# Optimization experiments

Measured on AMD Instinct MI355X. Metric: run time of the kernel, lower is better.

Reference implementation:

```python
import jax, jax.numpy as jnp
import numpy as np

B, N, D, E, MULT = 4, 512, 1024, 8, 4
H = D * MULT
CAPACITY_FACTOR = 1.0
EPSILON = 1e-6


def setup_inputs() -> dict:
    key = jax.random.key(0)
    ks = jax.random.split(key, 4)
    s1 = 1.0 / np.sqrt(D)
    s2 = 1.0 / np.sqrt(H)
    return {
        "x": jax.random.normal(ks[0], (B, N, D), jnp.float32),
        "w_gate": jax.random.uniform(ks[1], (D, E), jnp.float32, -s1, s1),
        "b_gate": jnp.zeros((E,), jnp.float32),
        "w1": jax.random.uniform(ks[2], (E, D, H), jnp.float32, -s1, s1),
        "b1": jnp.zeros((E, H), jnp.float32),
        "w2": jax.random.uniform(ks[3], (E, H, D), jnp.float32, -s2, s2),
        "b2": jnp.zeros((E, D), jnp.float32),
    }


def _cv_squared(v):
    # torch: x.float().var() is unbiased (ddof=1)
    eps = 1e-10
    m = jnp.mean(v)
    return jnp.var(v, ddof=1) / (m * m + eps)


def reference(x, w_gate, b_gate, w1, b1, w2, b2):
    b, n, d = x.shape
    e = w_gate.shape[1]
    capacity = float(int(CAPACITY_FACTOR * b))  # int(capacity_factor * x.size(0))

    # SwitchGate
    gate = jax.nn.softmax(x @ w_gate + b_gate, axis=-1)          # [B,N,E]
    top_idx = jnp.argmax(gate, axis=-1)                          # [B,N]  == topk(1) indices
    # faithful to torch scatter_(dim=1, top_k_indices, 1): mask[bi, idx[bi,ni,0], 0] = 1
    mask = jnp.zeros_like(gate).at[jnp.arange(b)[:, None], top_idx, 0].set(1.0)
    masked = gate * mask
    denom = masked.sum(0, keepdims=True) + EPSILON               # [1,N,E]
    gate_scores = masked / denom * capacity                      # [B,N,E]
    importance = gate_scores.sum(0)                              # [N,E]
    load = (gate_scores > 0).sum(0).astype(jnp.float32)          # [N,E]
    loss = _cv_squared(importance) + _cv_squared(load)

    # Experts: FeedForward(dim, dim, mult) = Linear -> GELU(exact) -> Linear, all E at once
    h = jax.nn.gelu(jnp.einsum('bnd,edh->bneh', x, w1) + b1, approximate=False)  # [B,N,E,H]
    expert_out = jnp.einsum('bneh,ehd->bned', h, w2) + b2                        # [B,N,E,D]

    # moe_output = sum(gate_scores.unsqueeze(-2) * stacked_expert_outputs, dim=-1)
    out = jnp.einsum('bne,bned->bnd', gate_scores, expert_out)                   # [B,N,D]
    return out, loss
```

## Files before the change

kernel.cpp:

```cpp
#include <hip/hip_runtime.h>
#include <math.h>

static constexpr int Bb = 4;
static constexpr int Nn = 512;
static constexpr int Dd = 1024;
static constexpr int Ee = 8;
static constexpr int Hh = 4096;
static constexpr float CAP = 4.0f;
static constexpr float EPS = 1e-6f;

static constexpr int P1S = 32;
static constexpr int P2S = 32;


__global__ __launch_bounds__(256) void k1_gate_ffn1(
    const float* __restrict__ x, const float* __restrict__ wg,
    const float* __restrict__ bg, const float* __restrict__ w1,
    int* __restrict__ bmask, float* __restrict__ gate0,
    float* __restrict__ p1, float* __restrict__ out)
{
    __shared__ float smem[8 * 1028 + 16];
    const int blk = blockIdx.x;
    const int tid = threadIdx.x;

    if (blk < 256) {
        const int hc = blk & 7, ks = blk >> 3, k0 = ks * 32;
        {
            const int t = tid >> 3, q = tid & 7;
            const int row = (t >> 3) * Nn + (t & 7);
            float4 v = *(const float4*)(x + (size_t)row * Dd + k0 + q * 4);
            smem[(q * 4 + 0) * 32 + t] = v.x;
            smem[(q * 4 + 1) * 32 + t] = v.y;
            smem[(q * 4 + 2) * 32 + t] = v.z;
            smem[(q * 4 + 3) * 32 + t] = v.w;
        }
        __syncthreads();
        const int h = hc * 512 + tid * 2;
        const float* wp = w1 + (size_t)k0 * Hh + h;
        float2 acc[32];
#pragma unroll
        for (int t = 0; t < 32; ++t) acc[t] = make_float2(0.f, 0.f);
#pragma unroll
        for (int half = 0; half < 2; ++half) {
            float2 wbuf[16];
#pragma unroll
            for (int kk = 0; kk < 16; ++kk)
                wbuf[kk] = *(const float2*)(wp + (size_t)(half * 16 + kk) * Hh);
#pragma unroll
            for (int kk = 0; kk < 16; ++kk) {
                const float4* xrow = (const float4*)(smem + (half * 16 + kk) * 32);
                const float2 w = wbuf[kk];
#pragma unroll
                for (int t4 = 0; t4 < 8; ++t4) {
                    float4 xv = xrow[t4];
                    acc[t4 * 4 + 0].x = fmaf(xv.x, w.x, acc[t4 * 4 + 0].x);
                    acc[t4 * 4 + 0].y = fmaf(xv.x, w.y, acc[t4 * 4 + 0].y);
                    acc[t4 * 4 + 1].x = fmaf(xv.y, w.x, acc[t4 * 4 + 1].x);
                    acc[t4 * 4 + 1].y = fmaf(xv.y, w.y, acc[t4 * 4 + 1].y);
                    acc[t4 * 4 + 2].x = fmaf(xv.z, w.x, acc[t4 * 4 + 2].x);
                    acc[t4 * 4 + 2].y = fmaf(xv.z, w.y, acc[t4 * 4 + 2].y);
                    acc[t4 * 4 + 3].x = fmaf(xv.w, w.x, acc[t4 * 4 + 3].x);
                    acc[t4 * 4 + 3].y = fmaf(xv.w, w.y, acc[t4 * 4 + 3].y);
                }
            }
        }
        float* o = p1 + ((size_t)ks * 32) * Hh + h;
#pragma unroll
        for (int t = 0; t < 32; ++t) { *(float2*)o = acc[t]; o += Hh; }
    } else if (blk < 512) {
        const int g = blk - 256;
        for (int i = tid; i < Dd * Ee; i += 256)
            smem[(i & 7) * 1028 + (i >> 3)] = wg[i];
        int* bb = (int*)&smem[8224];
        __syncthreads();
        const int wave = tid >> 6, lane = tid & 63;
        for (int j = 0; j < 2; ++j) {
            const int sub = wave + 4 * j;
            const int tok = g * 8 + sub;
            const float* xr = x + (size_t)tok * Dd;
            float acc[Ee];
#pragma unroll
            for (int e = 0; e < Ee; ++e) acc[e] = 0.f;
#pragma unroll
            for (int jj = 0; jj < 4; ++jj) {
                const int d0 = jj * 256 + lane * 4;
                float4 xv = *(const float4*)(xr + d0);
#pragma unroll
                for (int e = 0; e < Ee; ++e) {
                    float4 wv = *(const float4*)(&smem[e * 1028 + d0]);
                    acc[e] = fmaf(xv.x, wv.x, acc[e]);
                    acc[e] = fmaf(xv.y, wv.y, acc[e]);
                    acc[e] = fmaf(xv.z, wv.z, acc[e]);
                    acc[e] = fmaf(xv.w, wv.w, acc[e]);
                }
            }
#pragma unroll
            for (int e = 0; e < Ee; ++e) {
                float v = acc[e];
#pragma unroll
                for (int off = 32; off > 0; off >>= 1) v += __shfl_xor(v, off, 64);
                acc[e] = v + bg[e];
            }
            if (lane == 0) {
                int best = 0;
                float bv = acc[0];
#pragma unroll
                for (int e = 1; e < Ee; ++e)
                    if (acc[e] > bv) { bv = acc[e]; best = e; }
                bb[sub] = 1 << best;
                const int n = tok & (Nn - 1);
                const int b = tok >> 9;
                if (n < 8) {
                    float m = acc[0];
#pragma unroll
                    for (int e = 1; e < Ee; ++e) m = fmaxf(m, acc[e]);
                    float s = 0.f;
#pragma unroll
                    for (int e = 0; e < Ee; ++e) s += expf(acc[e] - m);
                    gate0[b * 8 + n] = expf(acc[0] - m) / s;
                }
            }
        }
        __syncthreads();
        if (tid == 0) {
            int m = 0;
#pragma unroll
            for (int i = 0; i < 8; ++i) m |= bb[i];
            bmask[g] = m;
        }
    } else {
        const int z = blk - 512;
        const float4 zero4 = make_float4(0.f, 0.f, 0.f, 0.f);
#pragma unroll
        for (int r = 0; r < 8; ++r) {
            const int row = z * 8 + r;
            const int n = row & (Nn - 1);
            if (n >= 8)
                *(float4*)(out + (size_t)row * Dd + tid * 4) = zero4;
        }
    }
}

__global__ __launch_bounds__(128) void k2_gelu_score(
    const float* __restrict__ p1, const float* __restrict__ b1,
    float* __restrict__ hT, const int* __restrict__ bmask,
    const float* __restrict__ gate0, float* __restrict__ gs,
    float* __restrict__ loss_out)
{
    const int blk = blockIdx.x, tid = threadIdx.x;
    if (blk < 256) {
        const int idx = blk * 128 + tid;
        const int hh0 = (idx << 2) & (Hh - 1);
        const int t = idx >> 10;
        float4 s = *(const float4*)(b1 + hh0);
#pragma unroll
        for (int q = 0; q < P1S; ++q) {
            float4 v = *(const float4*)(p1 + ((size_t)(q * 32 + t)) * Hh + hh0);
            s.x += v.x; s.y += v.y; s.z += v.z; s.w += v.w;
        }
        const float c = 0.70710678118654752440f;
        float4 r;
        r.x = 0.5f * s.x * (1.f + erff(s.x * c));
        r.y = 0.5f * s.y * (1.f + erff(s.y * c));
        r.z = 0.5f * s.z * (1.f + erff(s.z * c));
        r.w = 0.5f * s.w * (1.f + erff(s.w * c));
        *(float4*)(hT + (size_t)t * Hh + hh0) = r;
    } else if (tid < 64) {
        const int l = tid;
        int m0 = bmask[l], m1 = bmask[64 + l], m2 = bmask[128 + l], m3 = bmask[192 + l];
#pragma unroll
        for (int off = 32; off > 0; off >>= 1) {
            m0 |= __shfl_xor(m0, off, 64);
            m1 |= __shfl_xor(m1, off, 64);
            m2 |= __shfl_xor(m2, off, 64);
            m3 |= __shfl_xor(m3, off, 64);
        }
        float gm = 0.f;
        if (l < 32) {
            const int b = l >> 3, n = l & 7;
            const int sm = (b == 0) ? m0 : (b == 1) ? m1 : (b == 2) ? m2 : m3;
            if ((sm >> n) & 1) gm = gate0[l];
        }
        float den = gm + __shfl_xor(gm, 8, 64);
        den += __shfl_xor(den, 16, 64);
        float gsv = 0.f;
        if (l < 32) { gsv = gm / (den + EPS) * CAP; gs[l] = gsv; }
        float impn = gsv + __shfl_xor(gsv, 8, 64); impn += __shfl_xor(impn, 16, 64);
        float ldv = (gsv > 0.f) ? 1.f : 0.f;
        float ldn = ldv + __shfl_xor(ldv, 8, 64); ldn += __shfl_xor(ldn, 16, 64);
        float si = gsv, sl = ldv;
#pragma unroll
        for (int off = 32; off > 0; off >>= 1) {
            si += __shfl_xor(si, off, 64);
            sl += __shfl_xor(sl, off, 64);
        }
        const float M = (float)(Nn * Ee);
        const float mi = si / M, ml = sl / M;
        float di = (l < 8) ? (impn - mi) * (impn - mi) : 0.f;
        float dl = (l < 8) ? (ldn - ml) * (ldn - ml) : 0.f;
#pragma unroll
        for (int off = 32; off > 0; off >>= 1) {
            di += __shfl_xor(di, off, 64);
            dl += __shfl_xor(dl, off, 64);
        }
        if (l == 0) {
            di += (M - 8.f) * mi * mi;
            dl += (M - 8.f) * ml * ml;
            const float vi = di / (M - 1.f), vl = dl / (M - 1.f);
            *loss_out = vi / (mi * mi + 1e-10f) + vl / (ml * ml + 1e-10f);
        }
    }
}

__global__ __launch_bounds__(128) void k3_ffn2(
    const float* __restrict__ w2, const float* __restrict__ hT,
    float* __restrict__ p2)
{
    __shared__ float smem[128 * 32];
    const int tid = threadIdx.x;
    const int ky = blockIdx.y;
    {
        const int t = tid & 31, kq = tid >> 5;
        const float* src = hT + (size_t)t * Hh + ky * 128 + kq * 32;
#pragma unroll
        for (int c = 0; c < 8; ++c) {
            float4 v = *(const float4*)(src + c * 4);
            smem[(kq * 32 + c * 4 + 0) * 32 + t] = v.x;
            smem[(kq * 32 + c * 4 + 1) * 32 + t] = v.y;
            smem[(kq * 32 + c * 4 + 2) * 32 + t] = v.z;
            smem[(kq * 32 + c * 4 + 3) * 32 + t] = v.w;
        }
    }
    __syncthreads();
    const int d = blockIdx.x * 128 + tid;
    const int k0 = ky * 128;
    const float* wp = w2 + (size_t)k0 * Dd + d;
    float acc[32];
#pragma unroll
    for (int t = 0; t < 32; ++t) acc[t] = 0.f;
#pragma unroll
    for (int q = 0; q < 8; ++q) {
        float wbuf[16];
#pragma unroll
        for (int kk = 0; kk < 16; ++kk)
            wbuf[kk] = wp[(size_t)(q * 16 + kk) * Dd];
#pragma unroll
        for (int kk = 0; kk < 16; ++kk) {
            const float4* xrow = (const float4*)(smem + (q * 16 + kk) * 32);
            const float w = wbuf[kk];
#pragma unroll
            for (int t4 = 0; t4 < 8; ++t4) {
                float4 xv = xrow[t4];
                acc[t4 * 4 + 0] = fmaf(xv.x, w, acc[t4 * 4 + 0]);
                acc[t4 * 4 + 1] = fmaf(xv.y, w, acc[t4 * 4 + 1]);
                acc[t4 * 4 + 2] = fmaf(xv.z, w, acc[t4 * 4 + 2]);
                acc[t4 * 4 + 3] = fmaf(xv.w, w, acc[t4 * 4 + 3]);
            }
        }
    }
    float* o = p2 + ((size_t)ky * 32) * Dd + d;
#pragma unroll
    for (int t = 0; t < 32; ++t) { *o = acc[t]; o += Dd; }
}

__global__ __launch_bounds__(128) void k4_out(
    const float* __restrict__ p2, const float* __restrict__ b2,
    const float* __restrict__ gs, float* __restrict__ out)
{
    const int t = blockIdx.x >> 1;
    const int d4 = (blockIdx.x & 1) * 512 + threadIdx.x * 4;
    float4 a = make_float4(0.f, 0.f, 0.f, 0.f);
    const float* p = p2 + (size_t)t * Dd + d4;
#pragma unroll 8
    for (int s = 0; s < P2S; ++s) {
        float4 v = *(const float4*)p;
        p += (size_t)32 * Dd;
        a.x += v.x; a.y += v.y; a.z += v.z; a.w += v.w;
    }
    float4 bbv = *(const float4*)(b2 + d4);
    const float g = gs[t];
    const int b = t >> 3, n = t & 7;
    float4 o;
    o.x = g * (a.x + bbv.x);
    o.y = g * (a.y + bbv.y);
    o.z = g * (a.z + bbv.z);
    o.w = g * (a.w + bbv.w);
    *(float4*)(out + ((size_t)(b * Nn + n)) * Dd + d4) = o;
}

extern "C" void kernel_launch(void* const* d_in, const int* in_sizes, int n_in,
                              void* d_out, int out_size, void* d_ws, size_t ws_size,
                              hipStream_t stream) {
    const float* x  = (const float*)d_in[0];
    const float* wg = (const float*)d_in[1];
    const float* bg = (const float*)d_in[2];
    const float* w1 = (const float*)d_in[3];
    const float* b1 = (const float*)d_in[4];
    const float* w2 = (const float*)d_in[5];
    const float* b2 = (const float*)d_in[6];
    float* out = (float*)d_out;
    float* wsf = (float*)d_ws;

    int*   bmask = (int*)d_ws;
    float* gate0 = wsf + 256;
    float* gs    = wsf + 320;
    float* hT    = wsf + 512;
    float* p1    = wsf + 132096;
    float* p2    = wsf + 4326400;

    k1_gate_ffn1<<<dim3(768), dim3(256), 0, stream>>>(x, wg, bg, w1, bmask, gate0, p1, out);
    k2_gelu_score<<<dim3(257), dim3(128), 0, stream>>>(p1, b1, hT, bmask, gate0, gs,
                                                       out + (out_size - 1));
    k3_ffn2<<<dim3(8, 32), dim3(128), 0, stream>>>(w2, hT, p2);
    k4_out<<<dim3(64), dim3(128), 0, stream>>>(p2, b2, gs, out);
}
```

Before: 266.5 us.

## Replace split-K FFN1 with full-K register-prefetched tiles and fuse bias+GELU

After: 270.5 us. Within noise of the previous version (+1.5%).

```diff
diff --git a/kernel.cpp b/kernel.cpp
--- a/kernel.cpp
+++ b/kernel.cpp
@@ -1,7 +1,6 @@
 #include <hip/hip_runtime.h>
 #include <math.h>
 
-static constexpr int Bb = 4;
 static constexpr int Nn = 512;
 static constexpr int Dd = 1024;
 static constexpr int Ee = 8;
@@ -9,66 +8,110 @@
 static constexpr float CAP = 4.0f;
 static constexpr float EPS = 1e-6f;
 
-static constexpr int P1S = 32;
 static constexpr int P2S = 32;
 
 
-__global__ __launch_bounds__(256) void k1_gate_ffn1(
+__global__ __launch_bounds__(256) void n1_gate_ffn1(
     const float* __restrict__ x, const float* __restrict__ wg,
     const float* __restrict__ bg, const float* __restrict__ w1,
-    int* __restrict__ bmask, float* __restrict__ gate0,
-    float* __restrict__ p1, float* __restrict__ out)
+    const float* __restrict__ b1, int* __restrict__ bmask,
+    float* __restrict__ gate0, float* __restrict__ hT,
+    float* __restrict__ out)
 {
     __shared__ float smem[8 * 1028 + 16];
     const int blk = blockIdx.x;
     const int tid = threadIdx.x;
 
     if (blk < 256) {
-        const int hc = blk & 7, ks = blk >> 3, k0 = ks * 32;
+        float* sX = smem;
+        float* sW = smem + 2048;
+        const int hb = blk * 16;
+        const int h  = tid & 15;
+        const int tp = tid >> 4;
+        const int t0 = tid & 31, kq = tid >> 5;
+        const int row0 = (t0 >> 3) * Nn + (t0 & 7);
+        const int kwr  = tid >> 4;
+
+        float4 xr0, xr1;
+        float  wr[4];
         {
-            const int t = tid >> 3, q = tid & 7;
-            const int row = (t >> 3) * Nn + (t & 7);
-            float4 v = *(const float4*)(x + (size_t)row * Dd + k0 + q * 4);
-            smem[(q * 4 + 0) * 32 + t] = v.x;
-            smem[(q * 4 + 1) * 32 + t] = v.y;
-            smem[(q * 4 + 2) * 32 + t] = v.z;
-            smem[(q * 4 + 3) * 32 + t] = v.w;
+            const float* xp = x + (size_t)row0 * Dd;
+            xr0 = *(const float4*)(xp + kq * 4);
+            xr1 = *(const float4*)(xp + (kq + 8) * 4);
+#pragma unroll
+            for (int j = 0; j < 4; ++j)
+                wr[j] = w1[(size_t)(kwr + j * 16) * Hh + hb + h];
+        }
+        {
+            sX[(kq * 4 + 0) * 32 + t0] = xr0.x;
+            sX[(kq * 4 + 1) * 32 + t0] = xr0.y;
+            sX[(kq * 4 + 2) * 32 + t0] = xr0.z;
+            sX[(kq * 4 + 3) * 32 + t0] = xr0.w;
+            sX[((kq + 8) * 4 + 0) * 32 + t0] = xr1.x;
+            sX[((kq + 8) * 4 + 1) * 32 + t0] = xr1.y;
+            sX[((kq + 8) * 4 + 2) * 32 + t0] = xr1.z;
+            sX[((kq + 8) * 4 + 3) * 32 + t0] = xr1.w;
+#pragma unroll
+            for (int j = 0; j < 4; ++j)
+                sW[(kwr + j * 16) * 16 + h] = wr[j];
         }
         __syncthreads();
-        const int h = hc * 512 + tid * 2;
-        const float* wp = w1 + (size_t)k0 * Hh + h;
-        float2 acc[32];
-#pragma unroll
-        for (int t = 0; t < 32; ++t) acc[t] = make_float2(0.f, 0.f);
-#pragma unroll
-        for (int half = 0; half < 2; ++half) {
-            float2 wbuf[16];
-#pragma unroll
-            for (int kk = 0; kk < 16; ++kk)
-                wbuf[kk] = *(const float2*)(wp + (size_t)(half * 16 + kk) * Hh);
-#pragma unroll
-            for (int kk = 0; kk < 16; ++kk) {
-                const float4* xrow = (const float4*)(smem + (half * 16 + kk) * 32);
-                const float2 w = wbuf[kk];
-#pragma unroll
-                for (int t4 = 0; t4 < 8; ++t4) {
-                    float4 xv = xrow[t4];
-                    acc[t4 * 4 + 0].x = fmaf(xv.x, w.x, acc[t4 * 4 + 0].x);
-                    acc[t4 * 4 + 0].y = fmaf(xv.x, w.y, acc[t4 * 4 + 0].y);
-                    acc[t4 * 4 + 1].x = fmaf(xv.y, w.x, acc[t4 * 4 + 1].x);
-                    acc[t4 * 4 + 1].y = fmaf(xv.y, w.y, acc[t4 * 4 + 1].y);
-                    acc[t4 * 4 + 2].x = fmaf(xv.z, w.x, acc[t4 * 4 + 2].x);
-                    acc[t4 * 4 + 2].y = fmaf(xv.z, w.y, acc[t4 * 4 + 2].y);
-                    acc[t4 * 4 + 3].x = fmaf(xv.w, w.x, acc[t4 * 4 + 3].x);
-                    acc[t4 * 4 + 3].y = fmaf(xv.w, w.y, acc[t4 * 4 + 3].y);
-                }
-            }
-        }
-        float* o = p1 + ((size_t)ks * 32) * Hh + h;
-#pragma unroll
-        for (int t = 0; t < 32; ++t) { *(float2*)o = acc[t]; o += Hh; }
-    } else if (blk < 512) {
+
+        const float b1v = b1[hb + h];
+        float a0 = b1v, a1 = b1v;
+
+        for (int c = 0; c < 16; ++c) {
+            float4 nx0, nx1;
+            float  nw[4];
+            if (c < 15) {
+                const int k0 = (c + 1) * 64;
+                const float* xp = x + (size_t)row0 * Dd + k0;
+                nx0 = *(const float4*)(xp + kq * 4);
+                nx1 = *(const float4*)(xp + (kq + 8) * 4);
+#pragma unroll
+                for (int j = 0; j < 4; ++j)
+                    nw[j] = w1[(size_t)(k0 + kwr + j * 16) * Hh + hb + h];
+            }
+            const float* xp = sX + 2 * tp;
+#pragma unroll
+            for (int kk = 0; kk < 64; ++kk) {
+                const float  w  = sW[kk * 16 + h];
+                const float2 xv = *(const float2*)(xp + kk * 32);
+                a0 = fmaf(xv.x, w, a0);
+                a1 = fmaf(xv.y, w, a1);
+            }
+            if (c < 15) {
+                __syncthreads();
+                sX[(kq * 4 + 0) * 32 + t0] = nx0.x;
+                sX[(kq * 4 + 1) * 32 + t0] = nx0.y;
+                sX[(kq * 4 + 2) * 32 + t0] = nx0.z;
+                sX[(kq * 4 + 3) * 32 + t0] = nx0.w;
+                sX[((kq + 8) * 4 + 0) * 32 + t0] = nx1.x;
+                sX[((kq + 8) * 4 + 1) * 32 + t0] = nx1.y;
+                sX[((kq + 8) * 4 + 2) * 32 + t0] = nx1.z;
+                sX[((kq + 8) * 4 + 3) * 32 + t0] = nx1.w;
+#pragma unroll
+                for (int j = 0; j < 4; ++j)
+                    sW[((c + 1) * 64 ? (kwr + j * 16) : 0) * 16 + h] = nw[j];
+                __syncthreads();
+            }
+        }
+        const float cst = 0.70710678118654752440f;
+        const float g0 = 0.5f * a0 * (1.f + erff(a0 * cst));
+        const float g1 = 0.5f * a1 * (1.f + erff(a1 * cst));
+        hT[(size_t)(2 * tp) * Hh + hb + h]     = g0;
+        hT[(size_t)(2 * tp + 1) * Hh + hb + h] = g1;
+    } else {
         const int g = blk - 256;
+        {
+            const float4 zero4 = make_float4(0.f, 0.f, 0.f, 0.f);
+#pragma unroll
+            for (int r = 0; r < 8; ++r) {
+                const int tok = g * 8 + r;
+                if ((tok & (Nn - 1)) >= 8)
+                    *(float4*)(out + (size_t)tok * Dd + tid * 4) = zero4;
+            }
+        }
         for (int i = tid; i < Dd * Ee; i += 256)
             smem[(i & 7) * 1028 + (i >> 3)] = wg[i];
         int* bb = (int*)&smem[8224];
@@ -128,43 +171,61 @@
             for (int i = 0; i < 8; ++i) m |= bb[i];
             bmask[g] = m;
         }
-    } else {
-        const int z = blk - 512;
-        const float4 zero4 = make_float4(0.f, 0.f, 0.f, 0.f);
-#pragma unroll
-        for (int r = 0; r < 8; ++r) {
-            const int row = z * 8 + r;
-            const int n = row & (Nn - 1);
-            if (n >= 8)
-                *(float4*)(out + (size_t)row * Dd + tid * 4) = zero4;
-        }
     }
 }
 
-__global__ __launch_bounds__(128) void k2_gelu_score(
-    const float* __restrict__ p1, const float* __restrict__ b1,
-    float* __restrict__ hT, const int* __restrict__ bmask,
+__global__ __launch_bounds__(128) void n2_ffn2_score(
+    const float* __restrict__ w2, const float* __restrict__ hT,
+    float* __restrict__ p2, const int* __restrict__ bmask,
     const float* __restrict__ gate0, float* __restrict__ gs,
     float* __restrict__ loss_out)
 {
+    __shared__ float smem[128 * 32];
     const int blk = blockIdx.x, tid = threadIdx.x;
     if (blk < 256) {
-        const int idx = blk * 128 + tid;
-        const int hh0 = (idx << 2) & (Hh - 1);
-        const int t = idx >> 10;
-        float4 s = *(const float4*)(b1 + hh0);
-#pragma unroll
-        for (int q = 0; q < P1S; ++q) {
-            float4 v = *(const float4*)(p1 + ((size_t)(q * 32 + t)) * Hh + hh0);
-            s.x += v.x; s.y += v.y; s.z += v.z; s.w += v.w;
-        }
-        const float c = 0.70710678118654752440f;
-        float4 r;
-        r.x = 0.5f * s.x * (1.f + erff(s.x * c));
-        r.y = 0.5f * s.y * (1.f + erff(s.y * c));
-        r.z = 0.5f * s.z * (1.f + erff(s.z * c));
-        r.w = 0.5f * s.w * (1.f + erff(s.w * c));
-        *(float4*)(hT + (size_t)t * Hh + hh0) = r;
+        const int dx = blk & 7, ky = blk >> 3;
+        {
+            const int t = tid & 31, kq = tid >> 5;
+            const float* src = hT + (size_t)t * Hh + ky * 128 + kq * 32;
+#pragma unroll
+            for (int c = 0; c < 8; ++c) {
+                float4 v = *(const float4*)(src + c * 4);
+                smem[(kq * 32 + c * 4 + 0) * 32 + t] = v.x;
+                smem[(kq * 32 + c * 4 + 1) * 32 + t] = v.y;
+                smem[(kq * 32 + c * 4 + 2) * 32 + t] = v.z;
+                smem[(kq * 32 + c * 4 + 3) * 32 + t] = v.w;
+            }
+        }
+        __syncthreads();
+        const int d = dx * 128 + tid;
+        const int k0 = ky * 128;
+        const float* wp = w2 + (size_t)k0 * Dd + d;
+        float acc[32];
+#pragma unroll
+        for (int t = 0; t < 32; ++t) acc[t] = 0.f;
+#pragma unroll
+        for (int q = 0; q < 8; ++q) {
+            float wbuf[16];
+#pragma unroll
+            for (int kk = 0; kk < 16; ++kk)
+                wbuf[kk] = wp[(size_t)(q * 16 + kk) * Dd];
+#pragma unroll
+            for (int kk = 0; kk < 16; ++kk) {
+                const float4* xrow = (const float4*)(smem + (q * 16 + kk) * 32);
+                const float w = wbuf[kk];
+#pragma unroll
+                for (int t4 = 0; t4 < 8; ++t4) {
+                    float4 xv = xrow[t4];
+                    acc[t4 * 4 + 0] = fmaf(xv.x, w, acc[t4 * 4 + 0]);
+                    acc[t4 * 4 + 1] = fmaf(xv.y, w, acc[t4 * 4 + 1]);
+                    acc[t4 * 4 + 2] = fmaf(xv.z, w, acc[t4 * 4 + 2]);
+                    acc[t4 * 4 + 3] = fmaf(xv.w, w, acc[t4 * 4 + 3]);
+                }
+            }
+        }
+        float* o = p2 + ((size_t)ky * 32) * Dd + d;
+#pragma unroll
+        for (int t = 0; t < 32; ++t) { *o = acc[t]; o += Dd; }
     } else if (tid < 64) {
         const int l = tid;
         int m0 = bmask[l], m1 = bmask[64 + l], m2 = bmask[128 + l], m3 = bmask[192 + l];
@@ -212,58 +273,7 @@
     }
 }
 
-__global__ __launch_bounds__(128) void k3_ffn2(
-    const float* __restrict__ w2, const float* __restrict__ hT,
-    float* __restrict__ p2)
-{
-    __shared__ float smem[128 * 32];
-    const int tid = threadIdx.x;
-    const int ky = blockIdx.y;
-    {
-        const int t = tid & 31, kq = tid >> 5;
-        const float* src = hT + (size_t)t * Hh + ky * 128 + kq * 32;
-#pragma unroll
-        for (int c = 0; c < 8; ++c) {
-            float4 v = *(const float4*)(src + c * 4);
-            smem[(kq * 32 + c * 4 + 0) * 32 + t] = v.x;
-            smem[(kq * 32 + c * 4 + 1) * 32 + t] = v.y;
-            smem[(kq * 32 + c * 4 + 2) * 32 + t] = v.z;
-            smem[(kq * 32 + c * 4 + 3) * 32 + t] = v.w;
-        }
-    }
-    __syncthreads();
-    const int d = blockIdx.x * 128 + tid;
-    const int k0 = ky * 128;
-    const float* wp = w2 + (size_t)k0 * Dd + d;
-    float acc[32];
-#pragma unroll
-    for (int t = 0; t < 32; ++t) acc[t] = 0.f;
-#pragma unroll
-    for (int q = 0; q < 8; ++q) {
-        float wbuf[16];
-#pragma unroll
-        for (int kk = 0; kk < 16; ++kk)
-            wbuf[kk] = wp[(size_t)(q * 16 + kk) * Dd];
-#pragma unroll
-        for (int kk = 0; kk < 16; ++kk) {
-            const float4* xrow = (const float4*)(smem + (q * 16 + kk) * 32);
-            const float w = wbuf[kk];
-#pragma unroll
-            for (int t4 = 0; t4 < 8; ++t4) {
-                float4 xv = xrow[t4];
-                acc[t4 * 4 + 0] = fmaf(xv.x, w, acc[t4 * 4 + 0]);
-                acc[t4 * 4 + 1] = fmaf(xv.y, w, acc[t4 * 4 + 1]);
-                acc[t4 * 4 + 2] = fmaf(xv.z, w, acc[t4 * 4 + 2]);
-                acc[t4 * 4 + 3] = fmaf(xv.w, w, acc[t4 * 4 + 3]);
-            }
-        }
-    }
-    float* o = p2 + ((size_t)ky * 32) * Dd + d;
-#pragma unroll
-    for (int t = 0; t < 32; ++t) { *o = acc[t]; o += Dd; }
-}
-
-__global__ __launch_bounds__(128) void k4_out(
+__global__ __launch_bounds__(128) void n3_out(
     const float* __restrict__ p2, const float* __restrict__ b2,
     const float* __restrict__ gs, float* __restrict__ out)
 {
@@ -305,12 +315,11 @@
     float* gate0 = wsf + 256;
     float* gs    = wsf + 320;
     float* hT    = wsf + 512;
-    float* p1    = wsf + 132096;
-    float* p2    = wsf + 4326400;
-
-    k1_gate_ffn1<<<dim3(768), dim3(256), 0, stream>>>(x, wg, bg, w1, bmask, gate0, p1, out);
-    k2_gelu_score<<<dim3(257), dim3(128), 0, stream>>>(p1, b1, hT, bmask, gate0, gs,
+    float* p2    = wsf + 132096;
+
+    n1_gate_ffn1<<<dim3(512), dim3(256), 0, stream>>>(x, wg, bg, w1, b1, bmask,
+                                                      gate0, hT, out);
+    n2_ffn2_score<<<dim3(257), dim3(128), 0, stream>>>(w2, hT, p2, bmask, gate0, gs,
                                                        out + (out_size - 1));
-    k3_ffn2<<<dim3(8, 32), dim3(128), 0, stream>>>(w2, hT, p2);
-    k4_out<<<dim3(64), dim3(128), 0, stream>>>(p2, b2, gs, out);
+    n3_out<<<dim3(64), dim3(128), 0, stream>>>(p2, b2, gs, out);
 }
```

## Retile FFN2 split-K into finer slices with float4 weights and fold zero-fill into gate blocks

Applied to the files above, without the earlier changes.

After: 255.2 us. 1.04x faster.

```diff
diff --git a/kernel.cpp b/kernel.cpp
--- a/kernel.cpp
+++ b/kernel.cpp
@@ -1,7 +1,6 @@
 #include <hip/hip_runtime.h>
 #include <math.h>
 
-static constexpr int Bb = 4;
 static constexpr int Nn = 512;
 static constexpr int Dd = 1024;
 static constexpr int Ee = 8;
@@ -10,10 +9,10 @@
 static constexpr float EPS = 1e-6f;
 
 static constexpr int P1S = 32;
-static constexpr int P2S = 32;
-
-
-__global__ __launch_bounds__(256) void k1_gate_ffn1(
+static constexpr int P2S = 128;
+
+
+__global__ __launch_bounds__(256) void n1_gate_ffn1(
     const float* __restrict__ x, const float* __restrict__ wg,
     const float* __restrict__ bg, const float* __restrict__ w1,
     int* __restrict__ bmask, float* __restrict__ gate0,
@@ -67,8 +66,17 @@
         float* o = p1 + ((size_t)ks * 32) * Hh + h;
 #pragma unroll
         for (int t = 0; t < 32; ++t) { *(float2*)o = acc[t]; o += Hh; }
-    } else if (blk < 512) {
+    } else {
         const int g = blk - 256;
+        {
+            const float4 zero4 = make_float4(0.f, 0.f, 0.f, 0.f);
+#pragma unroll
+            for (int r = 0; r < 8; ++r) {
+                const int tok = g * 8 + r;
+                if ((tok & (Nn - 1)) >= 8)
+                    *(float4*)(out + (size_t)tok * Dd + tid * 4) = zero4;
+            }
+        }
         for (int i = tid; i < Dd * Ee; i += 256)
             smem[(i & 7) * 1028 + (i >> 3)] = wg[i];
         int* bb = (int*)&smem[8224];
@@ -128,20 +136,10 @@
             for (int i = 0; i < 8; ++i) m |= bb[i];
             bmask[g] = m;
         }
-    } else {
-        const int z = blk - 512;
-        const float4 zero4 = make_float4(0.f, 0.f, 0.f, 0.f);
-#pragma unroll
-        for (int r = 0; r < 8; ++r) {
-            const int row = z * 8 + r;
-            const int n = row & (Nn - 1);
-            if (n >= 8)
-                *(float4*)(out + (size_t)row * Dd + tid * 4) = zero4;
-        }
-    }
-}
-
-__global__ __launch_bounds__(128) void k2_gelu_score(
+    }
+}
+
+__global__ __launch_bounds__(128) void n2_gelu_score(
     const float* __restrict__ p1, const float* __restrict__ b1,
     float* __restrict__ hT, const int* __restrict__ bmask,
     const float* __restrict__ gate0, float* __restrict__ gs,
@@ -212,80 +210,86 @@
     }
 }
 
-__global__ __launch_bounds__(128) void k3_ffn2(
+__global__ __launch_bounds__(256) void n3_ffn2(
     const float* __restrict__ w2, const float* __restrict__ hT,
     float* __restrict__ p2)
 {
-    __shared__ float smem[128 * 32];
+    __shared__ float smem[32 * 32];
     const int tid = threadIdx.x;
-    const int ky = blockIdx.y;
+    const int dx = blockIdx.x & 3, ky = blockIdx.x >> 2;
+    const int k0 = ky * 32;
     {
-        const int t = tid & 31, kq = tid >> 5;
-        const float* src = hT + (size_t)t * Hh + ky * 128 + kq * 32;
-#pragma unroll
-        for (int c = 0; c < 8; ++c) {
-            float4 v = *(const float4*)(src + c * 4);
-            smem[(kq * 32 + c * 4 + 0) * 32 + t] = v.x;
-            smem[(kq * 32 + c * 4 + 1) * 32 + t] = v.y;
-            smem[(kq * 32 + c * 4 + 2) * 32 + t] = v.z;
-            smem[(kq * 32 + c * 4 + 3) * 32 + t] = v.w;
-        }
+        const int t = tid >> 3, c = tid & 7;
+        float4 v = *(const float4*)(hT + (size_t)t * Hh + k0 + c * 4);
+        smem[(c * 4 + 0) * 32 + t] = v.x;
+        smem[(c * 4 + 1) * 32 + t] = v.y;
+        smem[(c * 4 + 2) * 32 + t] = v.z;
+        smem[(c * 4 + 3) * 32 + t] = v.w;
     }
     __syncthreads();
-    const int d = blockIdx.x * 128 + tid;
-    const int k0 = ky * 128;
+    const int did = tid & 63;
+    const int tg  = tid >> 6;
+    const int d   = dx * 256 + did * 4;
     const float* wp = w2 + (size_t)k0 * Dd + d;
-    float acc[32];
-#pragma unroll
-    for (int t = 0; t < 32; ++t) acc[t] = 0.f;
-#pragma unroll
-    for (int q = 0; q < 8; ++q) {
-        float wbuf[16];
-#pragma unroll
-        for (int kk = 0; kk < 16; ++kk)
-            wbuf[kk] = wp[(size_t)(q * 16 + kk) * Dd];
-#pragma unroll
-        for (int kk = 0; kk < 16; ++kk) {
-            const float4* xrow = (const float4*)(smem + (q * 16 + kk) * 32);
-            const float w = wbuf[kk];
-#pragma unroll
-            for (int t4 = 0; t4 < 8; ++t4) {
-                float4 xv = xrow[t4];
-                acc[t4 * 4 + 0] = fmaf(xv.x, w, acc[t4 * 4 + 0]);
-                acc[t4 * 4 + 1] = fmaf(xv.y, w, acc[t4 * 4 + 1]);
-                acc[t4 * 4 + 2] = fmaf(xv.z, w, acc[t4 * 4 + 2]);
-                acc[t4 * 4 + 3] = fmaf(xv.w, w, acc[t4 * 4 + 3]);
-            }
-        }
-    }
-    float* o = p2 + ((size_t)ky * 32) * Dd + d;
-#pragma unroll
-    for (int t = 0; t < 32; ++t) { *o = acc[t]; o += Dd; }
-}
-
-__global__ __launch_bounds__(128) void k4_out(
+    float4 acc[8];
+#pragma unroll
+    for (int tt = 0; tt < 8; ++tt) acc[tt] = make_float4(0.f, 0.f, 0.f, 0.f);
+#pragma unroll
+    for (int bq = 0; bq < 4; ++bq) {
+        float4 wbuf[8];
+#pragma unroll
+        for (int kk = 0; kk < 8; ++kk)
+            wbuf[kk] = *(const float4*)(wp + (size_t)(bq * 8 + kk) * Dd);
+#pragma unroll
+        for (int kk = 0; kk < 8; ++kk) {
+            const float4 w4 = wbuf[kk];
+            const float* xr = smem + (bq * 8 + kk) * 32 + tg * 8;
+            const float4 x0 = *(const float4*)xr;
+            const float4 x1 = *(const float4*)(xr + 4);
+            acc[0].x = fmaf(x0.x, w4.x, acc[0].x); acc[0].y = fmaf(x0.x, w4.y, acc[0].y);
+            acc[0].z = fmaf(x0.x, w4.z, acc[0].z); acc[0].w = fmaf(x0.x, w4.w, acc[0].w);
+            acc[1].x = fmaf(x0.y, w4.x, acc[1].x); acc[1].y = fmaf(x0.y, w4.y, acc[1].y);
+            acc[1].z = fmaf(x0.y, w4.z, acc[1].z); acc[1].w = fmaf(x0.y, w4.w, acc[1].w);
+            acc[2].x = fmaf(x0.z, w4.x, acc[2].x); acc[2].y = fmaf(x0.z, w4.y, acc[2].y);
+            acc[2].z = fmaf(x0.z, w4.z, acc[2].z); acc[2].w = fmaf(x0.z, w4.w, acc[2].w);
+            acc[3].x = fmaf(x0.w, w4.x, acc[3].x); acc[3].y = fmaf(x0.w, w4.y, acc[3].y);
+            acc[3].z = fmaf(x0.w, w4.z, acc[3].z); acc[3].w = fmaf(x0.w, w4.w, acc[3].w);
+            acc[4].x = fmaf(x1.x, w4.x, acc[4].x); acc[4].y = fmaf(x1.x, w4.y, acc[4].y);
+            acc[4].z = fmaf(x1.x, w4.z, acc[4].z); acc[4].w = fmaf(x1.x, w4.w, acc[4].w);
+            acc[5].x = fmaf(x1.y, w4.x, acc[5].x); acc[5].y = fmaf(x1.y, w4.y, acc[5].y);
+            acc[5].z = fmaf(x1.y, w4.z, acc[5].z); acc[5].w = fmaf(x1.y, w4.w, acc[5].w);
+            acc[6].x = fmaf(x1.z, w4.x, acc[6].x); acc[6].y = fmaf(x1.z, w4.y, acc[6].y);
+            acc[6].z = fmaf(x1.z, w4.z, acc[6].z); acc[6].w = fmaf(x1.z, w4.w, acc[6].w);
+            acc[7].x = fmaf(x1.w, w4.x, acc[7].x); acc[7].y = fmaf(x1.w, w4.y, acc[7].y);
+            acc[7].z = fmaf(x1.w, w4.z, acc[7].z); acc[7].w = fmaf(x1.w, w4.w, acc[7].w);
+        }
+    }
+#pragma unroll
+    for (int tt = 0; tt < 8; ++tt)
+        *(float4*)(p2 + ((size_t)(ky * 32 + tg * 8 + tt)) * Dd + d) = acc[tt];
+}
+
+__global__ __launch_bounds__(256) void n4_out(
     const float* __restrict__ p2, const float* __restrict__ b2,
     const float* __restrict__ gs, float* __restrict__ out)
 {
     const int t = blockIdx.x >> 1;
-    const int d4 = (blockIdx.x & 1) * 512 + threadIdx.x * 4;
-    float4 a = make_float4(0.f, 0.f, 0.f, 0.f);
-    const float* p = p2 + (size_t)t * Dd + d4;
-#pragma unroll 8
+    const int d2 = (blockIdx.x & 1) * 512 + threadIdx.x * 2;
+    float2 a = make_float2(0.f, 0.f);
+    const float* p = p2 + (size_t)t * Dd + d2;
+#pragma unroll 16
     for (int s = 0; s < P2S; ++s) {
-        float4 v = *(const float4*)p;
+        float2 v = *(const float2*)p;
         p += (size_t)32 * Dd;
-        a.x += v.x; a.y += v.y; a.z += v.z; a.w += v.w;
-    }
-    float4 bbv = *(const float4*)(b2 + d4);
+        a.x += v.x; a.y += v.y;
+    }
+    float2 bbv = *(const float2*)(b2 + d2);
     const float g = gs[t];
     const int b = t >> 3, n = t & 7;
-    float4 o;
+    float2 o;
     o.x = g * (a.x + bbv.x);
     o.y = g * (a.y + bbv.y);
-    o.z = g * (a.z + bbv.z);
-    o.w = g * (a.w + bbv.w);
-    *(float4*)(out + ((size_t)(b * Nn + n)) * Dd + d4) = o;
+    *(float2*)(out + ((size_t)(b * Nn + n)) * Dd + d2) = o;
 }
 
 extern "C" void kernel_launch(void* const* d_in, const int* in_sizes, int n_in,
@@ -308,9 +312,10 @@
     float* p1    = wsf + 132096;
     float* p2    = wsf + 4326400;
 
-    k1_gate_ffn1<<<dim3(768), dim3(256), 0, stream>>>(x, wg, bg, w1, bmask, gate0, p1, out);
-    k2_gelu_score<<<dim3(257), dim3(128), 0, stream>>>(p1, b1, hT, bmask, gate0, gs,
+    n1_gate_ffn1<<<dim3(512), dim3(256), 0, stream>>>(x, wg, bg, w1, bmask, gate0,
+                                                      p1, out);
+    n2_gelu_score<<<dim3(257), dim3(128), 0, stream>>>(p1, b1, hT, bmask, gate0, gs,
                                                        out + (out_size - 1));
-    k3_ffn2<<<dim3(8, 32), dim3(128), 0, stream>>>(w2, hT, p2);
-    k4_out<<<dim3(64), dim3(128), 0, stream>>>(p2, b2, gs, out);
-}
+    n3_ffn2<<<dim3(512), dim3(256), 0, stream>>>(w2, hT, p2);
+    n4_out<<<dim3(64), dim3(256), 0, stream>>>(p2, b2, gs, out);
+}
```
